# Optimization experiments

Hardware: AMD Instinct MI355X
Metric: run time of the kernel (lower is better)

Reference implementation:

```python
import jax, jax.numpy as jnp
import numpy as np

# Hardware / quantization constants (DacAdcHardwareSettings + quant scales)
INPUT_BITS = 8
OUT_PREC_BITS = 8          # fractional precision bits of the ADC
OUT_RANGE_BITS = 4         # ADC full-scale range = 2**OUT_RANGE_BITS
VMAX = 0.6                 # DAC output voltage full scale
OUT_SCALE = 8020.0         # hardware_output_current_scaling (current -> ADC units)
INPUT_FACTOR = 0.15        # 1/(activation scale * quant_max)
OUTPUT_FACTOR = 0.01       # weight scale * activation scale * quant_max
G_SCALE = 1e-4             # conductance magnitude (Siemens) for memristor cells
WEIGHT_PRECISION = 4       # -> 3 bit-plane memristor arrays


def dac(x):
    # clamp to [-1,1], quantize to INPUT_BITS signed levels, scale to volts
    levels = 2.0 ** (INPUT_BITS - 1) - 1.0
    return VMAX * jnp.round(jnp.clip(x, -1.0, 1.0) * levels) / levels


def adc(current):
    # scale current to ADC units, quantize with fixed fractional step, clip to range
    step = 2.0 ** (-OUT_PREC_BITS)
    rng = 2.0 ** OUT_RANGE_BITS
    scaled = current * OUT_SCALE
    return jnp.clip(jnp.round(scaled / step) * step, -rng, rng)


def setup_inputs() -> dict:
    key = jax.random.key(0)
    k0, k1, k2, k3 = jax.random.split(key, 4)
    tokens, d_in, d_out = 8192, 4096, 4096
    n_planes = WEIGHT_PRECISION - 1
    x = jax.random.normal(k0, (tokens, d_in), dtype=jnp.float32)
    # paired memristor conductances per bit plane, input-major [plane, in, out]
    w_pos = jax.random.uniform(k1, (n_planes, d_in, d_out), dtype=jnp.float32) * G_SCALE
    w_neg = jax.random.uniform(k2, (n_planes, d_in, d_out), dtype=jnp.float32) * G_SCALE
    bias = jax.random.normal(k3, (d_out,), dtype=jnp.float32)
    return {"x": x, "w_pos": w_pos, "w_neg": w_neg, "bias": bias}


def reference(x, w_pos, w_neg, bias):
    # DAC: quantize scaled activations to drive voltages
    inp = dac(x * INPUT_FACTOR)                      # [B, I]
    # effective bit-plane weights: positive minus negative cell conductances
    w_eff = w_pos - w_neg                            # [P, I, O]
    # crossbar readout for all bit planes: I = V @ G
    planes = jnp.einsum('bi,pio->pbo', inp, w_eff)   # [P, B, O]
    q = adc(planes)                                  # quantized per plane
    # shift-accumulate: memristors[-1] is bit 0; memristors[i] (i<P-2) is bit P-2-i
    p = w_eff.shape[0]
    shifts = jnp.array([2.0 ** (p - 1 - i) for i in range(p)],
                       dtype=x.dtype)
    shifts = shifts.at[-1].set(1.0)                  # [4., 2., 1.] for precision 4
    mem_out = jnp.einsum('pbo,p->bo', q, shifts)
    return mem_out * OUTPUT_FACTOR + bias
```

## Files before the change

kernel.cpp:

```cpp
#include <hip/hip_runtime.h>
#include <hip/hip_bf16.h>
#include <stdint.h>

#define TOK  8192
#define DIN  4096
#define DOUT 4096
#define NPL  3

typedef unsigned short u16;
typedef __attribute__((ext_vector_type(8))) __bf16 bf16x8;
typedef __attribute__((ext_vector_type(4))) float f32x4;
typedef __attribute__((ext_vector_type(4))) unsigned short u16x4;

#define ADC_MUL   9699.7795275590551f
#define INV256    0.00390625f

#define GL(src, dst) __builtin_amdgcn_global_load_lds( \
    (const __attribute__((address_space(1))) void*)(src), \
    (__attribute__((address_space(3))) void*)(dst), 16, 0, 0)

__global__ void dac_kernel(const float* __restrict__ x, u16* __restrict__ a) {
    const int n4 = TOK * DIN / 4;
    int i = blockIdx.x * blockDim.x + threadIdx.x;
    const int stride = gridDim.x * blockDim.x;
    const float4* xv = (const float4*)x;
    u16x4* av = (u16x4*)a;
    for (; i < n4; i += stride) {
        float4 v = xv[i];
        u16x4 o;
        float t, k;
        t = v.x * 0.15f; t = fminf(1.0f, fmaxf(-1.0f, t)); k = rintf(t * 127.0f);
        o.x = (u16)(__float_as_uint(k) >> 16);
        t = v.y * 0.15f; t = fminf(1.0f, fmaxf(-1.0f, t)); k = rintf(t * 127.0f);
        o.y = (u16)(__float_as_uint(k) >> 16);
        t = v.z * 0.15f; t = fminf(1.0f, fmaxf(-1.0f, t)); k = rintf(t * 127.0f);
        o.z = (u16)(__float_as_uint(k) >> 16);
        t = v.w * 0.15f; t = fminf(1.0f, fmaxf(-1.0f, t)); k = rintf(t * 127.0f);
        o.w = (u16)(__float_as_uint(k) >> 16);
        av[i] = o;
    }
}

__global__ void wsplit_kernel(const float* __restrict__ wp, const float* __restrict__ wn,
                              u16* __restrict__ w) {
    __shared__ float tile[64][65];
    const int b   = blockIdx.x;
    const int p   = b >> 12;
    const int rem = b & 4095;
    const int ib  = rem >> 6, ob = rem & 63;
    const int t   = threadIdx.x;
    const size_t plane = (size_t)p * DIN * DOUT;

    {
        const int o4 = (t & 15) << 2;
        const int r0 = t >> 4;
#pragma unroll
        for (int pass = 0; pass < 4; ++pass) {
            const int r = (pass << 4) + r0;
            const size_t off = plane + (size_t)(ib * 64 + r) * DOUT + ob * 64 + o4;
            const float4 a = *(const float4*)(wp + off);
            const float4 c = *(const float4*)(wn + off);
            tile[r][o4 + 0] = a.x - c.x;
            tile[r][o4 + 1] = a.y - c.y;
            tile[r][o4 + 2] = a.z - c.z;
            tile[r][o4 + 3] = a.w - c.w;
        }
    }
    __syncthreads();
    const int lane = t & 63, w4 = t >> 6;
#pragma unroll
    for (int pass = 0; pass < 16; ++pass) {
        const int o = (pass << 2) + w4;
        float d = tile[lane][o];
        uint32_t db = __float_as_uint(d);
        uint32_t hb = (db + 0x7fffu + ((db >> 16) & 1u)) & 0xffff0000u;
        float l = d - __uint_as_float(hb);
        uint32_t lb = __float_as_uint(l);
        u16 lo16 = (u16)((lb + 0x7fffu + ((lb >> 16) & 1u)) >> 16);
        size_t base = (size_t)(ob * 64 + o) * 24576 + (size_t)p * 8192 + ib * 64 + lane;
        w[base] = (u16)(hb >> 16);
        w[base + 4096] = lo16;
    }
}

__global__ __launch_bounds__(512, 2) void gemm_kernel(
    const u16* __restrict__ A,
    const u16* __restrict__ W,
    const float* __restrict__ bias,
    float* __restrict__ out)
{
    __shared__ __align__(16) char lds[147456];

    const int bid = blockIdx.x;
    const int g   = ((bid & 7) << 7) | (bid >> 3);
    const int mblk = g & 31, nblk = g >> 5;
    const int row0 = mblk << 8, col0 = nblk << 7;

    const int tid = threadIdx.x;
    const int lane = tid & 63, wid = tid >> 6;
    const int wm = wid & 3, wn = wid >> 2;

    const int swzb = (((tid & 7) ^ ((tid >> 3) & 7)) << 4);
    const char* gA = (const char*)A;
    const char* gB = (const char*)W;
    const size_t aRow = (size_t)(row0 + (tid >> 3)) * (DIN * 2) + swzb;
    const size_t bRow = (size_t)(col0 + (tid >> 3)) * (24576 * 2) + swzb;
    const int dstL = wid << 10;

    const int offK0 = (((lane >> 4) + 0) ^ (lane & 7)) << 4;
    const int offK1 = (((lane >> 4) + 4) ^ (lane & 7)) << 4;
    const int aRdRow = ((wm << 6) + (lane & 15)) << 7;
    const int bRdRow = ((wn << 6) + (lane & 15)) << 7;

    f32x4 acc[4][4], fin[4][4];
#pragma unroll
    for (int i = 0; i < 4; ++i)
#pragma unroll
        for (int j = 0; j < 4; ++j) {
            acc[i][j] = (f32x4){0.f, 0.f, 0.f, 0.f};
            fin[i][j] = (f32x4){0.f, 0.f, 0.f, 0.f};
        }

    auto stage = [&](int tile, int part, int buf) {
        const size_t kB = (size_t)tile << 7;
        const size_t kA = (size_t)((tile & 63) << 7);
        char* la = lds + (buf << 15) + dstL;
        char* lb = lds + 98304 + (buf << 14) + dstL;
        if (part == 0) {
            GL(gA + aRow + kA,           la);
            GL(gA + aRow + kA + 524288,  la + 8192);
            GL(gB + bRow + kB,           lb);
        } else {
            GL(gA + aRow + kA + 1048576, la + 16384);
            GL(gA + aRow + kA + 1572864, la + 24576);
            GL(gB + bRow + kB + 3145728, lb + 8192);
        }
    };

    auto phase = [&](int aBuf, int bBuf, int offK, int stTile, int stPart, int stBuf,
                     bool doStage) {
        bf16x8 av[4], bv[4];
        const char* la = lds + aBuf + aRdRow + offK;
        const char* lb = lds + bBuf + bRdRow + offK;
#pragma unroll
        for (int mi = 0; mi < 4; ++mi) av[mi] = *(const bf16x8*)(la + (mi << 11));
#pragma unroll
        for (int ni = 0; ni < 4; ++ni) bv[ni] = *(const bf16x8*)(lb + (ni << 11));
        if (doStage) stage(stTile, stPart, stBuf);
        asm volatile("s_waitcnt lgkmcnt(0)" ::: "memory");
        __builtin_amdgcn_sched_barrier(0);
        __builtin_amdgcn_s_setprio(1);
#pragma unroll
        for (int mi = 0; mi < 4; ++mi)
#pragma unroll
            for (int ni = 0; ni < 4; ++ni)
                acc[mi][ni] = __builtin_amdgcn_mfma_f32_16x16x32_bf16(
                    av[mi], bv[ni], acc[mi][ni], 0, 0, 0);
        __builtin_amdgcn_s_setprio(0);
    };

    stage(0, 0, 0); stage(0, 1, 0);
    stage(1, 0, 1); stage(1, 1, 1);
    asm volatile("s_waitcnt vmcnt(6)" ::: "memory");
    __builtin_amdgcn_s_barrier();

    int bufc = 0;
    for (int kt = 0; kt < 384; ++kt) {
        const int nxt  = bufc ? bufc - 1 : 2;
        const int aBuf = bufc << 15;
        const int bBuf = 98304 + (bufc << 14);
        const bool st  = (kt < 382);
        phase(aBuf, bBuf, offK0, kt + 2, 0, nxt, st);
        phase(aBuf, bBuf, offK1, kt + 2, 1, nxt, st);
        if ((kt & 127) == 127) {
            const float sh = (kt < 128) ? 4.f : (kt < 256) ? 2.f : 1.f;
#pragma unroll
            for (int mi = 0; mi < 4; ++mi)
#pragma unroll
                for (int ni = 0; ni < 4; ++ni)
#pragma unroll
                    for (int r = 0; r < 4; ++r) {
                        float q = rintf(acc[mi][ni][r] * ADC_MUL) * INV256;
                        q = fminf(16.0f, fmaxf(-16.0f, q));
                        fin[mi][ni][r] += sh * q;
                        acc[mi][ni][r] = 0.f;
                    }
        }
        if (st) { asm volatile("s_waitcnt vmcnt(6)" ::: "memory"); }
        else    { asm volatile("s_waitcnt vmcnt(0)" ::: "memory"); }
        __builtin_amdgcn_s_barrier();
        bufc = (bufc == 2) ? 0 : bufc + 1;
    }

    const int orow0 = row0 + (wm << 6) + ((lane >> 4) << 2);
    const int ocol0 = col0 + (wn << 6) + (lane & 15);
#pragma unroll
    for (int ni = 0; ni < 4; ++ni) {
        const int c = ocol0 + (ni << 4);
        const float bv = bias[c];
#pragma unroll
        for (int mi = 0; mi < 4; ++mi)
#pragma unroll
            for (int r = 0; r < 4; ++r)
                out[(size_t)(orow0 + (mi << 4) + r) * DOUT + c] = fin[mi][ni][r] * 0.01f + bv;
    }
}

extern "C" void kernel_launch(void* const* d_in, const int* in_sizes, int n_in,
                              void* d_out, int out_size, void* d_ws, size_t ws_size,
                              hipStream_t stream) {
    const float* x    = (const float*)d_in[0];
    const float* wp   = (const float*)d_in[1];
    const float* wn   = (const float*)d_in[2];
    const float* bias = (const float*)d_in[3];
    float* out = (float*)d_out;

    u16* A = (u16*)d_ws;
    u16* W = A + (size_t)TOK * DIN;

    dac_kernel<<<dim3(4096), dim3(256), 0, stream>>>(x, A);
    wsplit_kernel<<<dim3(NPL * 64 * 64), dim3(256), 0, stream>>>(wp, wn, W);
    gemm_kernel<<<dim3(1024), dim3(512), 0, stream>>>(A, W, bias, out);
}
```

Before: 2.267 ms.

## Interleave weight hi/lo halves and reuse A fragments across both halves

The weight split kernel now stores the hi and lo bf16 halves of each 64-wide K chunk next to each other. This lets each GEMM iteration load one A tile and multiply it against both the hi and lo B tiles, so A fragments are read from LDS once and used twice. The main loop moves from a triple-buffered 384-step schedule to a double-buffered 192-step one, split into four phases with interleaved global-to-LDS staging and more barriers. This cuts LDS read traffic per MFMA and the LDS footprint, at the cost of less prefetch depth and more synchronisation points.

```diff
diff --git a/kernel.cpp b/kernel.cpp
--- a/kernel.cpp
+++ b/kernel.cpp
@@ -77,11 +77,33 @@
         float l = d - __uint_as_float(hb);
         uint32_t lb = __float_as_uint(l);
         u16 lo16 = (u16)((lb + 0x7fffu + ((lb >> 16) & 1u)) >> 16);
-        size_t base = (size_t)(ob * 64 + o) * 24576 + (size_t)p * 8192 + ib * 64 + lane;
-        w[base] = (u16)(hb >> 16);
-        w[base + 4096] = lo16;
-    }
-}
+        size_t base = (size_t)(ob * 64 + o) * 24576 + (size_t)p * 8192 + ib * 128 + lane;
+        w[base]      = (u16)(hb >> 16);
+        w[base + 64] = lo16;
+    }
+}
+
+#define PHASE(AREG, BOFF, KOFF, STAGE_STMT, WAIT_STMT)                                  \
+    {                                                                                   \
+        bf16x8 bR[4];                                                                   \
+        _Pragma("unroll")                                                               \
+        for (int ni = 0; ni < 4; ++ni)                                                  \
+            bR[ni] = *(const bf16x8*)(lB + (BOFF) + bRd + (ni << 11) + (KOFF));         \
+        STAGE_STMT;                                                                     \
+        __builtin_amdgcn_s_barrier();                                                   \
+        asm volatile("s_waitcnt lgkmcnt(0)" ::: "memory");                              \
+        __builtin_amdgcn_sched_barrier(0);                                              \
+        __builtin_amdgcn_s_setprio(1);                                                  \
+        _Pragma("unroll")                                                               \
+        for (int mi = 0; mi < 4; ++mi)                                                  \
+            _Pragma("unroll")                                                           \
+            for (int ni = 0; ni < 4; ++ni)                                              \
+                acc[mi][ni] = __builtin_amdgcn_mfma_f32_16x16x32_bf16(                  \
+                    AREG[mi], bR[ni], acc[mi][ni], 0, 0, 0);                            \
+        __builtin_amdgcn_s_setprio(0);                                                  \
+        WAIT_STMT;                                                                      \
+        __builtin_amdgcn_s_barrier();                                                   \
+    }
 
 __global__ __launch_bounds__(512, 2) void gemm_kernel(
     const u16* __restrict__ A,
@@ -89,28 +111,27 @@
     const float* __restrict__ bias,
     float* __restrict__ out)
 {
-    __shared__ __align__(16) char lds[147456];
+    __shared__ __align__(16) char lds[131072];
 
     const int bid = blockIdx.x;
     const int g   = ((bid & 7) << 7) | (bid >> 3);
     const int mblk = g & 31, nblk = g >> 5;
     const int row0 = mblk << 8, col0 = nblk << 7;
 
-    const int tid = threadIdx.x;
-    const int lane = tid & 63, wid = tid >> 6;
-    const int wm = wid & 3, wn = wid >> 2;
+    const int tid = threadIdx.x, lane = tid & 63, wid = tid >> 6;
+    const int wm = wid >> 1, wn = wid & 1;
 
     const int swzb = (((tid & 7) ^ ((tid >> 3) & 7)) << 4);
     const char* gA = (const char*)A;
     const char* gB = (const char*)W;
-    const size_t aRow = (size_t)(row0 + (tid >> 3)) * (DIN * 2) + swzb;
-    const size_t bRow = (size_t)(col0 + (tid >> 3)) * (24576 * 2) + swzb;
+    const size_t aRow = (size_t)(row0 + (tid >> 3)) * 8192 + swzb;
+    const size_t bRow = (size_t)(col0 + (tid >> 3)) * 49152 + swzb;
     const int dstL = wid << 10;
 
-    const int offK0 = (((lane >> 4) + 0) ^ (lane & 7)) << 4;
-    const int offK1 = (((lane >> 4) + 4) ^ (lane & 7)) << 4;
-    const int aRdRow = ((wm << 6) + (lane & 15)) << 7;
-    const int bRdRow = ((wn << 6) + (lane & 15)) << 7;
+    const int koff0 = (((lane >> 4) + 0) ^ (lane & 7)) << 4;
+    const int koff1 = (((lane >> 4) + 4) ^ (lane & 7)) << 4;
+    const int aRd = ((wm << 6) + (lane & 15)) << 7;
+    const int bRd = ((wn << 6) + (lane & 15)) << 7;
 
     f32x4 acc[4][4], fin[4][4];
 #pragma unroll
@@ -121,59 +142,60 @@
             fin[i][j] = (f32x4){0.f, 0.f, 0.f, 0.f};
         }
 
-    auto stage = [&](int tile, int part, int buf) {
-        const size_t kB = (size_t)tile << 7;
-        const size_t kA = (size_t)((tile & 63) << 7);
-        char* la = lds + (buf << 15) + dstL;
-        char* lb = lds + 98304 + (buf << 14) + dstL;
-        if (part == 0) {
-            GL(gA + aRow + kA,           la);
-            GL(gA + aRow + kA + 524288,  la + 8192);
-            GL(gB + bRow + kB,           lb);
-        } else {
-            GL(gA + aRow + kA + 1048576, la + 16384);
-            GL(gA + aRow + kA + 1572864, la + 24576);
-            GL(gB + bRow + kB + 3145728, lb + 8192);
-        }
+    auto stageA = [&](int it1, int j, char* dst) {
+        GL(gA + aRow + ((size_t)j << 19) + ((size_t)(it1 & 63) << 7),
+           dst + (j << 13) + dstL);
     };
-
-    auto phase = [&](int aBuf, int bBuf, int offK, int stTile, int stPart, int stBuf,
-                     bool doStage) {
-        bf16x8 av[4], bv[4];
-        const char* la = lds + aBuf + aRdRow + offK;
-        const char* lb = lds + bBuf + bRdRow + offK;
-#pragma unroll
-        for (int mi = 0; mi < 4; ++mi) av[mi] = *(const bf16x8*)(la + (mi << 11));
-#pragma unroll
-        for (int ni = 0; ni < 4; ++ni) bv[ni] = *(const bf16x8*)(lb + (ni << 11));
-        if (doStage) stage(stTile, stPart, stBuf);
-        asm volatile("s_waitcnt lgkmcnt(0)" ::: "memory");
-        __builtin_amdgcn_sched_barrier(0);
-        __builtin_amdgcn_s_setprio(1);
+    auto stageBhi = [&](int it1, int j, char* dst) {
+        GL(gB + bRow + (size_t)it1 * 256 + ((size_t)j << 6) * 49152,
+           dst + (j << 13) + dstL);
+    };
+    auto stageBlo = [&](int it1, int j, char* dst) {
+        GL(gB + bRow + (size_t)it1 * 256 + 128 + ((size_t)j << 6) * 49152,
+           dst + 16384 + (j << 13) + dstL);
+    };
+
+    {
+        char* a0 = lds;
+        char* b0 = lds + 65536;
+        stageA(0, 0, a0); stageA(0, 1, a0); stageA(0, 2, a0); stageA(0, 3, a0);
+        stageBhi(0, 0, b0); stageBhi(0, 1, b0);
+        stageBlo(0, 0, b0); stageBlo(0, 1, b0);
+        asm volatile("s_waitcnt vmcnt(2)" ::: "memory");
+        __builtin_amdgcn_s_barrier();
+    }
+
+    for (int it = 0; it < 192; ++it) {
+        const int buf = it & 1;
+        const char* lA = lds + (buf << 15);
+        const char* lB = lds + 65536 + (buf << 15);
+        char* sA1 = lds + ((buf ^ 1) << 15);
+        char* sB1 = lds + 65536 + ((buf ^ 1) << 15);
+        const bool st = (it < 191);
+
+        bf16x8 aR0[4], aR1[4];
 #pragma unroll
         for (int mi = 0; mi < 4; ++mi)
-#pragma unroll
-            for (int ni = 0; ni < 4; ++ni)
-                acc[mi][ni] = __builtin_amdgcn_mfma_f32_16x16x32_bf16(
-                    av[mi], bv[ni], acc[mi][ni], 0, 0, 0);
-        __builtin_amdgcn_s_setprio(0);
-    };
-
-    stage(0, 0, 0); stage(0, 1, 0);
-    stage(1, 0, 1); stage(1, 1, 1);
-    asm volatile("s_waitcnt vmcnt(6)" ::: "memory");
-    __builtin_amdgcn_s_barrier();
-
-    int bufc = 0;
-    for (int kt = 0; kt < 384; ++kt) {
-        const int nxt  = bufc ? bufc - 1 : 2;
-        const int aBuf = bufc << 15;
-        const int bBuf = 98304 + (bufc << 14);
-        const bool st  = (kt < 382);
-        phase(aBuf, bBuf, offK0, kt + 2, 0, nxt, st);
-        phase(aBuf, bBuf, offK1, kt + 2, 1, nxt, st);
-        if ((kt & 127) == 127) {
-            const float sh = (kt < 128) ? 4.f : (kt < 256) ? 2.f : 1.f;
+            aR0[mi] = *(const bf16x8*)(lA + aRd + (mi << 11) + koff0);
+#pragma unroll
+        for (int mi = 0; mi < 4; ++mi)
+            aR1[mi] = *(const bf16x8*)(lA + aRd + (mi << 11) + koff1);
+
+        PHASE(aR0, 0, koff0,
+              { if (st) { stageA(it + 1, 0, sA1); stageA(it + 1, 1, sA1); } }, {});
+        PHASE(aR1, 0, koff1,
+              { if (st) { stageA(it + 1, 2, sA1); stageA(it + 1, 3, sA1); } },
+              { if (st) asm volatile("s_waitcnt vmcnt(4)" ::: "memory");
+                else    asm volatile("s_waitcnt vmcnt(0)" ::: "memory"); });
+        PHASE(aR0, 16384, koff0,
+              { if (st) { stageBhi(it + 1, 0, sB1); stageBhi(it + 1, 1, sB1); } }, {});
+        PHASE(aR1, 16384, koff1,
+              { if (st) { stageBlo(it + 1, 0, sB1); stageBlo(it + 1, 1, sB1); } },
+              { if (st) asm volatile("s_waitcnt vmcnt(2)" ::: "memory");
+                else    asm volatile("s_waitcnt vmcnt(0)" ::: "memory"); });
+
+        if ((it & 63) == 63) {
+            const float sh = (it == 63) ? 4.f : (it == 127) ? 2.f : 1.f;
 #pragma unroll
             for (int mi = 0; mi < 4; ++mi)
 #pragma unroll
@@ -186,10 +208,6 @@
                         acc[mi][ni][r] = 0.f;
                     }
         }
-        if (st) { asm volatile("s_waitcnt vmcnt(6)" ::: "memory"); }
-        else    { asm volatile("s_waitcnt vmcnt(0)" ::: "memory"); }
-        __builtin_amdgcn_s_barrier();
-        bufc = (bufc == 2) ? 0 : bufc + 1;
     }
 
     const int orow0 = row0 + (wm << 6) + ((lane >> 4) << 2);
```

Result: faster. 1.861 ms (-17.9%).
